# Optimization experiments

Measured on AMD Instinct MI355X. Metric: run time of the kernel, lower is better.

## Reference

```python
import jax, jax.numpy as jnp
import numpy as np


def setup_inputs() -> dict:
    key = jax.random.key(0)
    ks = jax.random.split(key, 5)
    B, C, H, W = 4, 256, 64, 64
    Cq = C // 8
    x = jax.random.normal(ks[0], (B, C, H, W), dtype=jnp.float32)
    Wq = jax.random.normal(ks[1], (Cq, C), dtype=jnp.float32) * (1.0 / np.sqrt(C))
    Wk = jax.random.normal(ks[2], (Cq, C), dtype=jnp.float32) * (1.0 / np.sqrt(C))
    Wv = jax.random.normal(ks[3], (C, C), dtype=jnp.float32) * (1.0 / np.sqrt(C))
    bq = jnp.zeros((Cq,), dtype=jnp.float32)
    bk = jnp.zeros((Cq,), dtype=jnp.float32)
    bv = jnp.zeros((C,), dtype=jnp.float32)
    gamma = jnp.ones((1,), dtype=jnp.float32)
    return {"x": x, "Wq": Wq, "bq": bq, "Wk": Wk, "bk": bk, "Wv": Wv, "bv": bv, "gamma": gamma}


def reference(x, Wq, bq, Wk, bk, Wv, bv, gamma):
    B, C, H, W = x.shape
    N = H * W
    xf = x.reshape(B, C, N)                      # (B, C, N)
    # 1x1 convs == per-pixel linear projections over channels
    q = jnp.einsum('dc,bcn->bdn', Wq, xf) + bq[None, :, None]   # (B, C/8, N)
    k = jnp.einsum('dc,bcn->bdn', Wk, xf) + bk[None, :, None]   # (B, C/8, N)
    v = jnp.einsum('dc,bcn->bdn', Wv, xf) + bv[None, :, None]   # (B, C,   N)
    # attention: note original has NO 1/sqrt(d) scaling
    scores = jnp.einsum('bdn,bdm->bnm', q, k)     # (B, N, N)
    attn = jax.nn.softmax(scores, axis=-1)
    out = jnp.einsum('bnm,bdm->bnd', attn, v)     # (B, N, C)
    out = out.transpose(0, 2, 1).reshape(B, C, H, W)
    return gamma * out + x
```

## Files before the change

### kernel.cpp

```cpp
#include <hip/hip_runtime.h>

#define BATCH 4
#define CH    256
#define DQ    32
#define NPIX  4096

typedef unsigned short u16;
typedef unsigned int   u32;
typedef __attribute__((ext_vector_type(8))) short short8;
typedef __attribute__((ext_vector_type(16))) float f32x16;

__device__ __forceinline__ float b2f(u32 u) {
  union { u32 i; float f; } v; v.i = (u & 0xffffu) << 16; return v.f;
}
__device__ __forceinline__ u16 f2b(float f) {
  union { float f; u32 i; } v; v.f = f;
  u32 x = v.i; x += 0x7fffu + ((x >> 16) & 1u);
  return (u16)(x >> 16);
}

__global__ __launch_bounds__(256) void proj(
    const float* __restrict__ x,
    const float* __restrict__ Wq, const float* __restrict__ bq,
    const float* __restrict__ Wk, const float* __restrict__ bk,
    const float* __restrict__ Wv, const float* __restrict__ bv,
    u16* __restrict__ q_t, u16* __restrict__ k_t, u16* __restrict__ v_swz)
{
  const int nt = blockIdx.x, jt = blockIdx.y, b = blockIdx.z;
  const int t = threadIdx.x;
  const int w = t >> 6, lane = t & 63, hl = lane >> 5, l31 = lane & 31;
  const int n0 = nt * 128;

  __shared__ u16 wls[2][16 * 2 * 32 * 8];
  __shared__ u16 xls[2][128 * 24];
  __shared__ float bias_s[32];

  const float* Wsrc; const float* bsrc; int jrow0;
  if (jt == 0)      { Wsrc = Wq; bsrc = bq; jrow0 = 0; }
  else if (jt == 1) { Wsrc = Wk; bsrc = bk; jrow0 = 0; }
  else              { Wsrc = Wv; bsrc = bv; jrow0 = (jt - 2) * 32; }

  for (int i = 0; i < 32; ++i) {
    const int flat = i * 256 + t;
    const int j = flat >> 8, e = flat & 255;
    const float v = Wsrc[(size_t)(jrow0 + j) * CH + e];
    const u16 hi = f2b(v);
    const u16 lo = f2b(v - b2f(hi));
    const int idx = (((e >> 4) * 2 + ((e >> 3) & 1)) * 32 + j) * 8 + (e & 7);
    wls[0][idx] = hi; wls[1][idx] = lo;
  }
  if (t < 32) bias_s[t] = bsrc[jrow0 + t];

  f32x16 acc;
  #pragma unroll
  for (int r = 0; r < 16; ++r) acc[r] = 0.f;

  const int nn = t & 127, esub = (t >> 7) * 8;
  for (int kk = 0; kk < 16; ++kk) {
    __syncthreads();
    #pragma unroll
    for (int i2 = 0; i2 < 4; ++i2) {
      const int el = esub + 2 * i2;
      const float v0 = x[((size_t)b * CH + kk * 16 + el    ) * NPIX + n0 + nn];
      const float v1 = x[((size_t)b * CH + kk * 16 + el + 1) * NPIX + n0 + nn];
      const u16 h0 = f2b(v0), h1 = f2b(v1);
      const u16 lo0 = f2b(v0 - b2f(h0)), lo1 = f2b(v1 - b2f(h1));
      *(u32*)&xls[0][nn * 24 + el] = (u32)h0 | ((u32)h1 << 16);
      *(u32*)&xls[1][nn * 24 + el] = (u32)lo0 | ((u32)lo1 << 16);
    }
    __syncthreads();
    const short8 wa_h = *(const short8*)&wls[0][((kk * 2 + hl) * 32 + l31) * 8];
    const short8 wa_l = *(const short8*)&wls[1][((kk * 2 + hl) * 32 + l31) * 8];
    const int nb = w * 32 + l31;
    const short8 xb_h = *(const short8*)&xls[0][nb * 24 + hl * 8];
    const short8 xb_l = *(const short8*)&xls[1][nb * 24 + hl * 8];
    acc = __builtin_amdgcn_mfma_f32_32x32x16_bf16(wa_h, xb_h, acc, 0, 0, 0);
    acc = __builtin_amdgcn_mfma_f32_32x32x16_bf16(wa_h, xb_l, acc, 0, 0, 0);
    acc = __builtin_amdgcn_mfma_f32_32x32x16_bf16(wa_l, xb_h, acc, 0, 0, 0);
  }

  #pragma unroll
  for (int r = 0; r < 16; ++r)
    acc[r] += bias_s[(r & 3) + 8 * (r >> 2) + 4 * hl];

  if (jt <= 1) {
    u16* dst = (jt == 0) ? q_t : k_t;
    const int n = n0 + w * 32 + l31;
    #pragma unroll
    for (int r2 = 0; r2 < 4; ++r2) {
      uint2 pk;
      pk.x = (u32)f2b(acc[4 * r2 + 0]) | ((u32)f2b(acc[4 * r2 + 1]) << 16);
      pk.y = (u32)f2b(acc[4 * r2 + 2]) | ((u32)f2b(acc[4 * r2 + 3]) << 16);
      *(uint2*)(dst + ((size_t)b * NPIX + n) * DQ + 4 * hl + 8 * r2) = pk;
    }
  } else {
    const int mc = nt * 4 + w;
    const int kc = (l31 >> 4) & 1, h3 = (l31 >> 3) & 1, j8 = l31 & 7;
    u16* dst = v_swz + (((((size_t)b * 128 + mc) * 8 + (jt - 2)) * 2 + kc) * 2 + h3) * 256 + j8;
    #pragma unroll
    for (int r = 0; r < 16; ++r) {
      const int c5 = (r & 3) + 8 * (r >> 2) + 4 * hl;
      dst[c5 * 8] = f2b(acc[r]);
    }
  }
}

__global__ __launch_bounds__(256, 2) void attn(
    const u16* __restrict__ q_t, const u16* __restrict__ k_t,
    const u16* __restrict__ v_swz, const float* __restrict__ x,
    const float* __restrict__ gamma, float* __restrict__ out)
{
  const int b = blockIdx.y, t = threadIdx.x;
  const int w = t >> 6, lane = t & 63, hl = lane >> 5, l31 = lane & 31;
  const int n0 = blockIdx.x * 32;

  __shared__ float cbuf[8192];
  __shared__ float lbuf[4][64];

  short8 qf[2];
  #pragma unroll
  for (int kd = 0; kd < 2; ++kd)
    qf[kd] = *(const short8*)(q_t + ((size_t)b * NPIX + n0 + l31) * DQ + kd * 16 + hl * 8);

  f32x16 acc[8];
  #pragma unroll
  for (int ct = 0; ct < 8; ++ct)
    #pragma unroll
    for (int r = 0; r < 16; ++r) acc[ct][r] = 0.f;
  float lrun = 0.f;

  for (int cc = 0; cc < 32; ++cc) {
    const int mc = w * 32 + cc;

    const short8 kf0 = *(const short8*)(k_t + ((size_t)b * NPIX + mc * 32 + l31) * DQ + hl * 8);
    const short8 kf1 = *(const short8*)(k_t + ((size_t)b * NPIX + mc * 32 + l31) * DQ + 16 + hl * 8);
    f32x16 st;
    #pragma unroll
    for (int r = 0; r < 16; ++r) st[r] = 0.f;
    st = __builtin_amdgcn_mfma_f32_32x32x16_bf16(kf0, qf[0], st, 0, 0, 0);
    st = __builtin_amdgcn_mfma_f32_32x32x16_bf16(kf1, qf[1], st, 0, 0, 0);

    u32 pk[4][2];
    #pragma unroll
    for (int g = 0; g < 4; ++g) {
      const float e0 = __expf(st[4 * g + 0]);
      const float e1 = __expf(st[4 * g + 1]);
      const float e2 = __expf(st[4 * g + 2]);
      const float e3 = __expf(st[4 * g + 3]);
      lrun += (e0 + e1) + (e2 + e3);
      pk[g][0] = (u32)f2b(e0) | ((u32)f2b(e1) << 16);
      pk[g][1] = (u32)f2b(e2) | ((u32)f2b(e3) << 16);
    }

    const size_t vbase = ((size_t)b * 128 + mc) * 8192;
    #pragma unroll
    for (int kc = 0; kc < 2; ++kc) {
      const u32 s0 = hl ? pk[2 * kc][0] : pk[2 * kc + 1][0];
      const u32 s1 = hl ? pk[2 * kc][1] : pk[2 * kc + 1][1];
      const u32 r0 = (u32)__shfl_xor((int)s0, 32);
      const u32 r1 = (u32)__shfl_xor((int)s1, 32);
      union { uint4 u; short8 s; } bu;
      bu.u.x = hl ? r0 : pk[2 * kc][0];
      bu.u.y = hl ? r1 : pk[2 * kc][1];
      bu.u.z = hl ? pk[2 * kc + 1][0] : r0;
      bu.u.w = hl ? pk[2 * kc + 1][1] : r1;
      #pragma unroll
      for (int ct = 0; ct < 8; ++ct) {
        const short8 av = *(const short8*)(v_swz + vbase + (size_t)(((ct * 2 + kc) * 2 + hl) * 256) + l31 * 8);
        acc[ct] = __builtin_amdgcn_mfma_f32_32x32x16_bf16(av, bu.s, acc[ct], 0, 0, 0);
      }
    }
  }

  lbuf[w][lane] = lrun;
  __syncthreads();
  for (int src = 1; src < 4; ++src) {
    if (w == src) {
      #pragma unroll
      for (int ct = 0; ct < 8; ++ct)
        #pragma unroll
        for (int r = 0; r < 16; ++r)
          cbuf[(ct * 16 + r) * 64 + lane] = acc[ct][r];
    }
    __syncthreads();
    if (w == 0) {
      #pragma unroll
      for (int ct = 0; ct < 8; ++ct)
        #pragma unroll
        for (int r = 0; r < 16; ++r)
          acc[ct][r] += cbuf[(ct * 16 + r) * 64 + lane];
    }
    __syncthreads();
  }

  if (w == 0) {
    float l = (lbuf[0][lane] + lbuf[1][lane]) + (lbuf[2][lane] + lbuf[3][lane]);
    l += __shfl_xor(l, 32);
    const float linv = 1.0f / l;
    const float g = gamma[0];
    #pragma unroll
    for (int ct = 0; ct < 8; ++ct)
      #pragma unroll
      for (int r = 0; r < 16; ++r) {
        const int c = ct * 32 + (r & 3) + 8 * (r >> 2) + 4 * hl;
        const size_t idx = ((size_t)b * CH + c) * NPIX + n0 + l31;
        out[idx] = g * acc[ct][r] * linv + x[idx];
      }
  }
}

extern "C" void kernel_launch(void* const* d_in, const int* in_sizes, int n_in,
                              void* d_out, int out_size, void* d_ws, size_t ws_size,
                              hipStream_t stream) {
  const float* x  = (const float*)d_in[0];
  const float* Wq = (const float*)d_in[1];
  const float* bq = (const float*)d_in[2];
  const float* Wk = (const float*)d_in[3];
  const float* bk = (const float*)d_in[4];
  const float* Wv = (const float*)d_in[5];
  const float* bv = (const float*)d_in[6];
  const float* gm = (const float*)d_in[7];
  float* out = (float*)d_out;

  const size_t qk_elems = (size_t)BATCH * NPIX * DQ;
  const size_t v_elems  = (size_t)BATCH * NPIX * CH;
  const size_t need = (2 * qk_elems + v_elems) * sizeof(u16);
  if (ws_size < need) return;

  u16* q_t   = (u16*)d_ws;
  u16* k_t   = q_t + qk_elems;
  u16* v_swz = k_t + qk_elems;

  proj<<<dim3(32, 10, BATCH), 256, 0, stream>>>(x, Wq, bq, Wk, bk, Wv, bv, q_t, k_t, v_swz);
  attn<<<dim3(NPIX / 32, BATCH), 256, 0, stream>>>(q_t, k_t, v_swz, x, gm, out);
}
```

Baseline: 163.0 us.

## Pre-swizzle weights, restructure projection per pixel tile, widen attention to 64 queries

Adds a small kernel that converts the weights to swizzled bf16 once per call instead of in every projection block. The projection kernel now loads each 32-pixel x tile once and computes Q, K and all V channel tiles from it across 8 waves. V uses hi-only bf16 instead of the split hi/lo scheme. The attention kernel moves to 512 threads covering 64 query pixels; probabilities are exchanged through double-buffered LDS so each V fragment load feeds two query tiles, and the cross-wave reduction is a tree. This cuts repeated x and V global loads at the cost of extra syncthreads per key chunk and lower V precision.

```diff
diff --git a/kernel.cpp b/kernel.cpp
--- a/kernel.cpp
+++ b/kernel.cpp
@@ -19,121 +19,141 @@
   return (u16)(x >> 16);
 }
 
-__global__ __launch_bounds__(256) void proj(
+__global__ __launch_bounds__(256) void wconv(
+    const float* __restrict__ Wq, const float* __restrict__ Wk,
+    const float* __restrict__ Wv, u16* __restrict__ wsz, u16* __restrict__ wsz_lo)
+{
+  const int blk = blockIdx.x;
+  const int jt = blk >> 4, kk = blk & 15;
+  #pragma unroll
+  for (int rep = 0; rep < 2; ++rep) {
+    const int idx = rep * 256 + threadIdx.x;
+    const int j = idx >> 4, el = idx & 15, e = kk * 16 + el;
+    const float* Wsrc = (jt == 0) ? Wq : (jt == 1) ? Wk : Wv;
+    const int row = (jt <= 1) ? j : (jt - 2) * 32 + j;
+    const float v = Wsrc[(size_t)row * CH + e];
+    const u16 hi = f2b(v);
+    const int o = (((jt * 16 + kk) * 2 + (el >> 3)) * 32 + j) * 8 + (el & 7);
+    wsz[o] = hi;
+    if (jt < 2) wsz_lo[o] = f2b(v - b2f(hi));
+  }
+}
+
+__global__ __launch_bounds__(512, 2) void proj(
     const float* __restrict__ x,
-    const float* __restrict__ Wq, const float* __restrict__ bq,
-    const float* __restrict__ Wk, const float* __restrict__ bk,
-    const float* __restrict__ Wv, const float* __restrict__ bv,
+    const u16* __restrict__ wsz, const u16* __restrict__ wsz_lo,
+    const float* __restrict__ bq, const float* __restrict__ bk, const float* __restrict__ bv,
     u16* __restrict__ q_t, u16* __restrict__ k_t, u16* __restrict__ v_swz)
 {
-  const int nt = blockIdx.x, jt = blockIdx.y, b = blockIdx.z;
+  const int b = blockIdx.y, nt = blockIdx.x;
+  const int n0 = nt * 32;
   const int t = threadIdx.x;
   const int w = t >> 6, lane = t & 63, hl = lane >> 5, l31 = lane & 31;
-  const int n0 = nt * 128;
-
-  __shared__ u16 wls[2][16 * 2 * 32 * 8];
-  __shared__ u16 xls[2][128 * 24];
-  __shared__ float bias_s[32];
-
-  const float* Wsrc; const float* bsrc; int jrow0;
-  if (jt == 0)      { Wsrc = Wq; bsrc = bq; jrow0 = 0; }
-  else if (jt == 1) { Wsrc = Wk; bsrc = bk; jrow0 = 0; }
-  else              { Wsrc = Wv; bsrc = bv; jrow0 = (jt - 2) * 32; }
-
-  for (int i = 0; i < 32; ++i) {
-    const int flat = i * 256 + t;
-    const int j = flat >> 8, e = flat & 255;
-    const float v = Wsrc[(size_t)(jrow0 + j) * CH + e];
-    const u16 hi = f2b(v);
-    const u16 lo = f2b(v - b2f(hi));
-    const int idx = (((e >> 4) * 2 + ((e >> 3) & 1)) * 32 + j) * 8 + (e & 7);
-    wls[0][idx] = hi; wls[1][idx] = lo;
-  }
-  if (t < 32) bias_s[t] = bsrc[jrow0 + t];
-
-  f32x16 acc;
-  #pragma unroll
-  for (int r = 0; r < 16; ++r) acc[r] = 0.f;
-
-  const int nn = t & 127, esub = (t >> 7) * 8;
-  for (int kk = 0; kk < 16; ++kk) {
-    __syncthreads();
-    #pragma unroll
-    for (int i2 = 0; i2 < 4; ++i2) {
-      const int el = esub + 2 * i2;
-      const float v0 = x[((size_t)b * CH + kk * 16 + el    ) * NPIX + n0 + nn];
-      const float v1 = x[((size_t)b * CH + kk * 16 + el + 1) * NPIX + n0 + nn];
-      const u16 h0 = f2b(v0), h1 = f2b(v1);
-      const u16 lo0 = f2b(v0 - b2f(h0)), lo1 = f2b(v1 - b2f(h1));
-      *(u32*)&xls[0][nn * 24 + el] = (u32)h0 | ((u32)h1 << 16);
-      *(u32*)&xls[1][nn * 24 + el] = (u32)lo0 | ((u32)lo1 << 16);
-    }
-    __syncthreads();
-    const short8 wa_h = *(const short8*)&wls[0][((kk * 2 + hl) * 32 + l31) * 8];
-    const short8 wa_l = *(const short8*)&wls[1][((kk * 2 + hl) * 32 + l31) * 8];
-    const int nb = w * 32 + l31;
-    const short8 xb_h = *(const short8*)&xls[0][nb * 24 + hl * 8];
-    const short8 xb_l = *(const short8*)&xls[1][nb * 24 + hl * 8];
-    acc = __builtin_amdgcn_mfma_f32_32x32x16_bf16(wa_h, xb_h, acc, 0, 0, 0);
-    acc = __builtin_amdgcn_mfma_f32_32x32x16_bf16(wa_h, xb_l, acc, 0, 0, 0);
-    acc = __builtin_amdgcn_mfma_f32_32x32x16_bf16(wa_l, xb_h, acc, 0, 0, 0);
-  }
-
-  #pragma unroll
-  for (int r = 0; r < 16; ++r)
-    acc[r] += bias_s[(r & 3) + 8 * (r >> 2) + 4 * hl];
-
-  if (jt <= 1) {
-    u16* dst = (jt == 0) ? q_t : k_t;
-    const int n = n0 + w * 32 + l31;
-    #pragma unroll
-    for (int r2 = 0; r2 < 4; ++r2) {
-      uint2 pk;
-      pk.x = (u32)f2b(acc[4 * r2 + 0]) | ((u32)f2b(acc[4 * r2 + 1]) << 16);
-      pk.y = (u32)f2b(acc[4 * r2 + 2]) | ((u32)f2b(acc[4 * r2 + 3]) << 16);
-      *(uint2*)(dst + ((size_t)b * NPIX + n) * DQ + 4 * hl + 8 * r2) = pk;
-    }
-  } else {
-    const int mc = nt * 4 + w;
-    const int kc = (l31 >> 4) & 1, h3 = (l31 >> 3) & 1, j8 = l31 & 7;
-    u16* dst = v_swz + (((((size_t)b * 128 + mc) * 8 + (jt - 2)) * 2 + kc) * 2 + h3) * 256 + j8;
-    #pragma unroll
-    for (int r = 0; r < 16; ++r) {
-      const int c5 = (r & 3) + 8 * (r >> 2) + 4 * hl;
-      dst[c5 * 8] = f2b(acc[r]);
-    }
-  }
-}
-
-__global__ __launch_bounds__(256, 2) void attn(
+
+  __shared__ __align__(16) u16 xh[32 * 264];
+  __shared__ __align__(16) u16 xl[32 * 264];
+
+  #pragma unroll
+  for (int i = 0; i < 4; ++i) {
+    const int e = i * 64 + (t >> 3), n4 = t & 7;
+    const float4 v4 = *(const float4*)&x[((size_t)b * CH + e) * NPIX + n0 + n4 * 4];
+    const float vv[4] = {v4.x, v4.y, v4.z, v4.w};
+    #pragma unroll
+    for (int jj = 0; jj < 4; ++jj) {
+      const u16 hi = f2b(vv[jj]);
+      xh[(n4 * 4 + jj) * 264 + e] = hi;
+      xl[(n4 * 4 + jj) * 264 + e] = f2b(vv[jj] - b2f(hi));
+    }
+  }
+  __syncthreads();
+
+  const int cnt[8] = {1, 1, 1, 1, 2, 2, 1, 1};
+  const int j0a[8] = {0, 1, 2, 4, 6, 8, 3, 5};
+  const int j1a[8] = {-1, -1, -1, -1, 7, 9, -1, -1};
+
+  for (int ii = 0; ii < cnt[w]; ++ii) {
+    const int jt = (ii == 0) ? j0a[w] : j1a[w];
+    f32x16 acc;
+    #pragma unroll
+    for (int r = 0; r < 16; ++r) acc[r] = 0.f;
+
+    if (jt <= 1) {
+      #pragma unroll
+      for (int kk = 0; kk < 16; ++kk) {
+        const int wo = ((jt * 16 + kk) * 2 + hl) * 256 + l31 * 8;
+        const short8 Ah = *(const short8*)&wsz[wo];
+        const short8 Al = *(const short8*)&wsz_lo[wo];
+        const int xo = l31 * 264 + kk * 16 + hl * 8;
+        const short8 Bh = *(const short8*)&xh[xo];
+        const short8 Bl = *(const short8*)&xl[xo];
+        acc = __builtin_amdgcn_mfma_f32_32x32x16_bf16(Ah, Bh, acc, 0, 0, 0);
+        acc = __builtin_amdgcn_mfma_f32_32x32x16_bf16(Ah, Bl, acc, 0, 0, 0);
+        acc = __builtin_amdgcn_mfma_f32_32x32x16_bf16(Al, Bh, acc, 0, 0, 0);
+      }
+    } else {
+      #pragma unroll
+      for (int kk = 0; kk < 16; ++kk) {
+        const short8 Ah = *(const short8*)&wsz[((jt * 16 + kk) * 2 + hl) * 256 + l31 * 8];
+        const short8 Bh = *(const short8*)&xh[l31 * 264 + kk * 16 + hl * 8];
+        acc = __builtin_amdgcn_mfma_f32_32x32x16_bf16(Ah, Bh, acc, 0, 0, 0);
+      }
+    }
+
+    if (jt <= 1) {
+      u16* dst = (jt == 0) ? q_t : k_t;
+      const float* bias = (jt == 0) ? bq : bk;
+      const int n = n0 + l31;
+      #pragma unroll
+      for (int r = 0; r < 16; ++r) {
+        const int d = (r & 3) + 8 * (r >> 2) + 4 * hl;
+        dst[((size_t)b * NPIX + n) * DQ + d] = f2b(acc[r] + bias[d]);
+      }
+    } else {
+      const int ctv = jt - 2;
+      const int kc = (l31 >> 4) & 1, h3 = (l31 >> 3) & 1, j8 = l31 & 7;
+      const size_t base = ((((size_t)b * 128 + nt) * 8 + ctv) * 2 + kc) * 2 + h3;
+      #pragma unroll
+      for (int r = 0; r < 16; ++r) {
+        const int c5 = (r & 3) + 8 * (r >> 2) + 4 * hl;
+        v_swz[base * 256 + c5 * 8 + j8] = f2b(acc[r] + bv[ctv * 32 + c5]);
+      }
+    }
+  }
+}
+
+__global__ __launch_bounds__(512, 2) void attn(
     const u16* __restrict__ q_t, const u16* __restrict__ k_t,
     const u16* __restrict__ v_swz, const float* __restrict__ x,
     const float* __restrict__ gamma, float* __restrict__ out)
 {
   const int b = blockIdx.y, t = threadIdx.x;
   const int w = t >> 6, lane = t & 63, hl = lane >> 5, l31 = lane & 31;
-  const int n0 = blockIdx.x * 32;
-
-  __shared__ float cbuf[8192];
-  __shared__ float lbuf[4][64];
+  const int mq = w & 3, ch = w >> 2;
+  const int n0 = blockIdx.x * 64;
+
+  __shared__ __align__(16) char smem[32768 + 2048];
+  uint4* plds = (uint4*)smem;
+  float* cbuf = (float*)smem;
+  float* lbuf = (float*)(smem + 32768);
 
   short8 qf[2];
   #pragma unroll
   for (int kd = 0; kd < 2; ++kd)
-    qf[kd] = *(const short8*)(q_t + ((size_t)b * NPIX + n0 + l31) * DQ + kd * 16 + hl * 8);
+    qf[kd] = *(const short8*)(q_t + ((size_t)b * NPIX + n0 + ch * 32 + l31) * DQ + kd * 16 + hl * 8);
 
   f32x16 acc[8];
   #pragma unroll
-  for (int ct = 0; ct < 8; ++ct)
-    #pragma unroll
-    for (int r = 0; r < 16; ++r) acc[ct][r] = 0.f;
+  for (int a = 0; a < 8; ++a)
+    #pragma unroll
+    for (int r = 0; r < 16; ++r) acc[a][r] = 0.f;
   float lrun = 0.f;
 
   for (int cc = 0; cc < 32; ++cc) {
-    const int mc = w * 32 + cc;
-
-    const short8 kf0 = *(const short8*)(k_t + ((size_t)b * NPIX + mc * 32 + l31) * DQ + hl * 8);
-    const short8 kf1 = *(const short8*)(k_t + ((size_t)b * NPIX + mc * 32 + l31) * DQ + 16 + hl * 8);
+    const int mc = mq * 32 + cc;
+
+    const u16* kp = k_t + ((size_t)b * NPIX + mc * 32 + l31) * DQ + hl * 8;
+    const short8 kf0 = *(const short8*)(kp);
+    const short8 kf1 = *(const short8*)(kp + 16);
     f32x16 st;
     #pragma unroll
     for (int r = 0; r < 16; ++r) st[r] = 0.f;
@@ -152,60 +172,95 @@
       pk[g][1] = (u32)f2b(e2) | ((u32)f2b(e3) << 16);
     }
 
-    const size_t vbase = ((size_t)b * 128 + mc) * 8192;
+    uint4 bown[2];
     #pragma unroll
     for (int kc = 0; kc < 2; ++kc) {
       const u32 s0 = hl ? pk[2 * kc][0] : pk[2 * kc + 1][0];
       const u32 s1 = hl ? pk[2 * kc][1] : pk[2 * kc + 1][1];
       const u32 r0 = (u32)__shfl_xor((int)s0, 32);
       const u32 r1 = (u32)__shfl_xor((int)s1, 32);
-      union { uint4 u; short8 s; } bu;
-      bu.u.x = hl ? r0 : pk[2 * kc][0];
-      bu.u.y = hl ? r1 : pk[2 * kc][1];
-      bu.u.z = hl ? pk[2 * kc + 1][0] : r0;
-      bu.u.w = hl ? pk[2 * kc + 1][1] : r1;
-      #pragma unroll
-      for (int ct = 0; ct < 8; ++ct) {
-        const short8 av = *(const short8*)(v_swz + vbase + (size_t)(((ct * 2 + kc) * 2 + hl) * 256) + l31 * 8);
-        acc[ct] = __builtin_amdgcn_mfma_f32_32x32x16_bf16(av, bu.s, acc[ct], 0, 0, 0);
-      }
-    }
-  }
-
-  lbuf[w][lane] = lrun;
+      bown[kc].x = hl ? r0 : pk[2 * kc][0];
+      bown[kc].y = hl ? r1 : pk[2 * kc][1];
+      bown[kc].z = hl ? pk[2 * kc + 1][0] : r0;
+      bown[kc].w = hl ? pk[2 * kc + 1][1] : r1;
+    }
+
+    short8 av[4][2];
+    const size_t vbase = ((size_t)b * 128 + mc) * 8192;
+    #pragma unroll
+    for (int ct = 0; ct < 4; ++ct)
+      #pragma unroll
+      for (int kc = 0; kc < 2; ++kc)
+        av[ct][kc] = *(const short8*)(v_swz + vbase +
+                       (size_t)((((ch * 4 + ct) * 2 + kc) * 2 + hl) * 256 + l31 * 8));
+
+    const int buf = cc & 1;
+    plds[(((buf * 4 + mq) * 2 + ch) * 2 + 0) * 64 + lane] = bown[0];
+    plds[(((buf * 4 + mq) * 2 + ch) * 2 + 1) * 64 + lane] = bown[1];
+    __syncthreads();
+    union { uint4 u; short8 s; } bu[2][2];
+    #pragma unroll
+    for (int nt = 0; nt < 2; ++nt)
+      #pragma unroll
+      for (int kc = 0; kc < 2; ++kc)
+        bu[nt][kc].u = plds[(((buf * 4 + mq) * 2 + nt) * 2 + kc) * 64 + lane];
+
+    #pragma unroll
+    for (int kc = 0; kc < 2; ++kc)
+      #pragma unroll
+      for (int ct = 0; ct < 4; ++ct)
+        #pragma unroll
+        for (int nt = 0; nt < 2; ++nt)
+          acc[nt * 4 + ct] =
+            __builtin_amdgcn_mfma_f32_32x32x16_bf16(av[ct][kc], bu[nt][kc].s, acc[nt * 4 + ct], 0, 0, 0);
+  }
+
+  lbuf[w * 64 + lane] = lrun;
   __syncthreads();
-  for (int src = 1; src < 4; ++src) {
-    if (w == src) {
-      #pragma unroll
-      for (int ct = 0; ct < 8; ++ct)
-        #pragma unroll
-        for (int r = 0; r < 16; ++r)
-          cbuf[(ct * 16 + r) * 64 + lane] = acc[ct][r];
-    }
-    __syncthreads();
-    if (w == 0) {
-      #pragma unroll
-      for (int ct = 0; ct < 8; ++ct)
-        #pragma unroll
-        for (int r = 0; r < 16; ++r)
-          acc[ct][r] += cbuf[(ct * 16 + r) * 64 + lane];
-    }
-    __syncthreads();
-  }
-
-  if (w == 0) {
-    float l = (lbuf[0][lane] + lbuf[1][lane]) + (lbuf[2][lane] + lbuf[3][lane]);
-    l += __shfl_xor(l, 32);
-    const float linv = 1.0f / l;
+
+  const int srcs[3] = {1, 3, 2}, dsts[3] = {0, 2, 0};
+  #pragma unroll
+  for (int h = 0; h < 2; ++h) {
+    for (int rnd = 0; rnd < 3; ++rnd) {
+      if (mq == srcs[rnd]) {
+        #pragma unroll
+        for (int ct = 0; ct < 4; ++ct)
+          #pragma unroll
+          for (int r = 0; r < 16; ++r)
+            cbuf[ch * 4096 + (ct * 16 + r) * 64 + lane] = acc[h * 4 + ct][r];
+      }
+      __syncthreads();
+      if (mq == dsts[rnd]) {
+        #pragma unroll
+        for (int ct = 0; ct < 4; ++ct)
+          #pragma unroll
+          for (int r = 0; r < 16; ++r)
+            acc[h * 4 + ct][r] += cbuf[ch * 4096 + (ct * 16 + r) * 64 + lane];
+      }
+      __syncthreads();
+    }
+  }
+
+  if (mq == 0) {
+    float linv[2];
+    #pragma unroll
+    for (int nt = 0; nt < 2; ++nt) {
+      float l = (lbuf[(nt * 4 + 0) * 64 + lane] + lbuf[(nt * 4 + 1) * 64 + lane])
+              + (lbuf[(nt * 4 + 2) * 64 + lane] + lbuf[(nt * 4 + 3) * 64 + lane]);
+      l += __shfl_xor(l, 32);
+      linv[nt] = 1.0f / l;
+    }
     const float g = gamma[0];
     #pragma unroll
-    for (int ct = 0; ct < 8; ++ct)
-      #pragma unroll
-      for (int r = 0; r < 16; ++r) {
-        const int c = ct * 32 + (r & 3) + 8 * (r >> 2) + 4 * hl;
-        const size_t idx = ((size_t)b * CH + c) * NPIX + n0 + l31;
-        out[idx] = g * acc[ct][r] * linv + x[idx];
-      }
+    for (int nt = 0; nt < 2; ++nt)
+      #pragma unroll
+      for (int ct = 0; ct < 4; ++ct)
+        #pragma unroll
+        for (int r = 0; r < 16; ++r) {
+          const int c = (ch * 4 + ct) * 32 + (r & 3) + 8 * (r >> 2) + 4 * hl;
+          const size_t idx = ((size_t)b * CH + c) * NPIX + n0 + nt * 32 + l31;
+          out[idx] = g * acc[nt * 4 + ct][r] * linv[nt] + x[idx];
+        }
   }
 }
 
@@ -222,15 +277,20 @@
   const float* gm = (const float*)d_in[7];
   float* out = (float*)d_out;
 
-  const size_t qk_elems = (size_t)BATCH * NPIX * DQ;
-  const size_t v_elems  = (size_t)BATCH * NPIX * CH;
-  const size_t need = (2 * qk_elems + v_elems) * sizeof(u16);
+  const size_t qk_e = (size_t)BATCH * NPIX * DQ;
+  const size_t v_e  = (size_t)BATCH * NPIX * CH;
+  const size_t w_e  = 10 * 16 * 2 * 32 * 8;
+  const size_t wl_e = 2 * 16 * 2 * 32 * 8;
+  const size_t need = (2 * qk_e + v_e + w_e + wl_e) * sizeof(u16);
   if (ws_size < need) return;
 
-  u16* q_t   = (u16*)d_ws;
-  u16* k_t   = q_t + qk_elems;
-  u16* v_swz = k_t + qk_elems;
-
-  proj<<<dim3(32, 10, BATCH), 256, 0, stream>>>(x, Wq, bq, Wk, bk, Wv, bv, q_t, k_t, v_swz);
-  attn<<<dim3(NPIX / 32, BATCH), 256, 0, stream>>>(q_t, k_t, v_swz, x, gm, out);
-}
+  u16* q_t    = (u16*)d_ws;
+  u16* k_t    = q_t + qk_e;
+  u16* v_swz  = k_t + qk_e;
+  u16* wsz    = v_swz + v_e;
+  u16* wsz_lo = wsz + w_e;
+
+  wconv<<<dim3(160), 256, 0, stream>>>(Wq, Wk, Wv, wsz, wsz_lo);
+  proj <<<dim3(NPIX / 32, BATCH), 512, 0, stream>>>(x, wsz, wsz_lo, bq, bk, bv, q_t, k_t, v_swz);
+  attn <<<dim3(NPIX / 64, BATCH), 512, 0, stream>>>(q_t, k_t, v_swz, x, gm, out);
+}
```

New measurement: 185.0 us. 1.14x slower.
